# Kernel tuning notes

Measured on AMD Instinct MI355X. Metric: run time of the kernel, lower is better.

Reference implementation:

```python
import jax, jax.numpy as jnp
import numpy as np

HEADS = 8
EPS = 1e-12  # F.normalize default eps


def conv1x1(t, w):
    # t: (B, Cin, H, W); w: (Cout, Cin) -> (B, Cout, H, W)
    return jnp.einsum('bchw,oc->bohw', t, w)


def cosine_attn(q, k, v, scale):
    # q: (B,h,d,Nq); k,v: (B,h,d,Nk). Cosine attention: L2-normalize over feature dim d.
    q = q / jnp.maximum(jnp.linalg.norm(q, axis=2, keepdims=True), EPS)
    k = k / jnp.maximum(jnp.linalg.norm(k, axis=2, keepdims=True), EPS)
    attn = jnp.einsum('bhdq,bhdk->bhqk', q, k) * scale
    attn = jax.nn.softmax(attn, axis=-1)
    return jnp.einsum('bhqk,bhdk->bhdq', attn, v)  # (B,h,d,Nq)


def setup_inputs() -> dict:
    key = jax.random.key(0)
    ks = jax.random.split(key, 8)
    B, C, H, W, L = 8, 512, 64, 64, 16
    def w(k, o, i):
        return jax.random.normal(k, (o, i), dtype=jnp.float32) * (1.0 / np.sqrt(i))
    return {
        'x': jax.random.normal(ks[0], (B, C, H, W), dtype=jnp.float32),
        'latents': jax.random.normal(ks[1], (1, C, 1, L), dtype=jnp.float32) * 0.02,
        'w_q_lat': w(ks[2], C, C),
        'w_kv_x': w(ks[3], 2 * C, C),
        'w_q_x': w(ks[4], C, C),
        'w_kv_lat': w(ks[5], 2 * C, C),
        'w_proj': w(ks[6], C, C),
        'b_proj': jnp.zeros((C,), dtype=jnp.float32),
    }


def reference(x, latents, w_q_lat, w_kv_x, w_q_x, w_kv_lat, w_proj, b_proj):
    B, C, H, W = x.shape
    L = latents.shape[-1]
    h = HEADS
    d = C // h
    scale = d ** (-0.5)

    # latents read from spatial features (compression)
    lat = jnp.broadcast_to(latents, (B, C, 1, L))
    ql = conv1x1(lat, w_q_lat).reshape(B, h, d, L)
    kvx = conv1x1(x, w_kv_x)
    kx = kvx[:, :C].reshape(B, h, d, H * W)
    vx = kvx[:, C:].reshape(B, h, d, H * W)
    lat_read = cosine_attn(ql, kx, vx, scale).reshape(B, C, 1, L)

    # latents write back into features (expansion)
    qx = conv1x1(x, w_q_x).reshape(B, h, d, H * W)
    kvl = conv1x1(lat_read, w_kv_lat)
    kl = kvl[:, :C].reshape(B, h, d, L)
    vl = kvl[:, C:].reshape(B, h, d, L)
    x_write = cosine_attn(qx, kl, vl, scale).reshape(B, C, H, W)

    # output projection (dropout p=0 -> identity)
    return conv1x1(x_write, w_proj) + b_proj[None, :, None, None]
```

## Files before the change

### kernel.cpp

```cpp
#include <hip/hip_runtime.h>


typedef __bf16 bf16x8 __attribute__((ext_vector_type(8)));
typedef float floatx4 __attribute__((ext_vector_type(4)));
typedef short short8_t __attribute__((ext_vector_type(8)));
typedef short short4_t __attribute__((ext_vector_type(4)));

#define DEV __device__ __forceinline__

DEV float bf2f(unsigned short u){ union{unsigned int i; float f;} v; v.i = ((unsigned int)u)<<16; return v.f; }
DEV unsigned short f2bf(float f){
  __bf16 h = (__bf16)f;
  unsigned short u; __builtin_memcpy(&u, &h, 2); return u;
}

DEV void glds16(const void* g, void* l){
  __builtin_amdgcn_global_load_lds((const __attribute__((address_space(1))) void*)g,
                                   (__attribute__((address_space(3))) void*)l, 16, 0, 0);
}

#define OFF_XT     256ull
#define OFF_KVX    (OFF_XT + 33554432ull)
#define OFF_WKVX   (OFF_KVX + 67108864ull)
#define OFF_WQX    (OFF_WKVX + 1048576ull)
#define OFF_WKVL   (OFF_WQX + 524288ull)
#define OFF_WPROJ  (OFF_WKVL + 1048576ull)
#define OFF_WQLAT  (OFF_WPROJ + 524288ull)
#define OFF_LATF   (OFF_WQLAT + 524288ull)
#define OFF_BIAS   (OFF_LATF + 32768ull)
#define OFF_QLH    (OFF_BIAS + 4096ull)
#define OFF_GNUM   (OFF_QLH + 32768ull)
#define OFF_GDEN   (OFF_GNUM + 524288ull)
#define OFF_KVL    (OFF_GDEN + 4096ull)
#define OFF_KHAT   (OFF_KVL + 524288ull)
#define OFF_GVL    (OFF_KHAT + 524288ull)

__global__ void k_sniff(const unsigned short* __restrict__ x, int* flag){
  int t = threadIdx.x;
  int m = 0;
  for (int i = t; i < 4096; i += 256){ int e = (x[i]>>7)&0xFF; m = (e>m)?e:m; }
  __shared__ int red[256];
  red[t] = m; __syncthreads();
  for (int s = 128; s > 0; s >>= 1){ if (t < s) red[t] = (red[t+s]>red[t])?red[t+s]:red[t]; __syncthreads(); }
  if (t == 0) flag[0] = (red[0] > 150) ? 1 : 0;
}

__global__ __launch_bounds__(256) void k_prep(const void* s0, const void* s1, const void* s2,
                                              const void* s3, const void* s4,
                                              const void* slat, const void* sbias,
                                              unsigned short* __restrict__ wdst,
                                              float* __restrict__ latf, float* __restrict__ biasf,
                                              float* __restrict__ zro,
                                              const int* __restrict__ flag){
  int b = blockIdx.x, t = threadIdx.x;
  int isf = *flag;
  if (b < 896){
    int e = b*2048 + t*8;
    const void* src; int off;
    if (e < 524288)      { src = s0; off = e; }
    else if (e < 786432) { src = s1; off = e - 524288; }
    else if (e < 1310720){ src = s2; off = e - 786432; }
    else if (e < 1572864){ src = s3; off = e - 1310720; }
    else                 { src = s4; off = e - 1572864; }
    if (isf){
      const float* s = (const float*)src + off;
      float4 v0 = *(const float4*)(s);
      float4 v1 = *(const float4*)(s+4);
      unsigned short tmp[8] __attribute__((aligned(16)));
      tmp[0]=f2bf(v0.x); tmp[1]=f2bf(v0.y); tmp[2]=f2bf(v0.z); tmp[3]=f2bf(v0.w);
      tmp[4]=f2bf(v1.x); tmp[5]=f2bf(v1.y); tmp[6]=f2bf(v1.z); tmp[7]=f2bf(v1.w);
      *(short8_t*)&wdst[e] = *(short8_t*)tmp;
    } else {
      *(short8_t*)&wdst[e] = *(const short8_t*)((const unsigned short*)src + off);
    }
  } else if (b < 900){
    int i = (b-896)*2048 + t*8;
#pragma unroll
    for (int j = 0; j < 8; ++j)
      latf[i+j] = isf ? ((const float*)slat)[i+j] : bf2f(((const unsigned short*)slat)[i+j]);
  } else if (b == 900){
    if (t < 512) biasf[t] = isf ? ((const float*)sbias)[t] : bf2f(((const unsigned short*)sbias)[t]);
    if (t + 256 < 512) biasf[t+256] = isf ? ((const float*)sbias)[t+256] : bf2f(((const unsigned short*)sbias)[t+256]);
  } else {
    int i = (b-901)*256 + t;
    float4 z; z.x=0.f; z.y=0.f; z.z=0.f; z.w=0.f;
    ((float4*)zro)[i] = z;
  }
}

__global__ __launch_bounds__(256) void k_xt(const void* __restrict__ xraw, unsigned short* __restrict__ xT,
                                            const int* __restrict__ flag){
  int nb = blockIdx.x, cb = blockIdx.y, b = blockIdx.z;
  int n0 = nb*64, c0 = cb*64;
  __shared__ unsigned short tile[64][72];
  int t = threadIdx.x;
  if (*flag){
    const float* xp = (const float*)xraw;
#pragma unroll
    for (int i = 0; i < 4; ++i){
      int ch = i*256 + t; int c = ch>>4, n4 = (ch&15)*4;
      float4 v = *(const float4*)&xp[((size_t)(b*512 + c0 + c))*4096 + n0 + n4];
      int cc = n4 ^ (((c>>3)&7)<<3);
      tile[c][cc+0]=f2bf(v.x); tile[c][cc+1]=f2bf(v.y); tile[c][cc+2]=f2bf(v.z); tile[c][cc+3]=f2bf(v.w);
    }
  } else {
    const unsigned short* xp = (const unsigned short*)xraw;
#pragma unroll
    for (int i = 0; i < 2; ++i){
      int ch = i*256 + t; int c = ch>>3, n8 = (ch&7)*8;
      *(short8_t*)&tile[c][n8 ^ (((c>>3)&7)<<3)] =
        *(const short8_t*)&xp[((size_t)(b*512 + c0 + c))*4096 + n0 + n8];
    }
  }
  __syncthreads();
#pragma unroll
  for (int i = 0; i < 2; ++i){
    int ch = i*256 + t; int n = ch>>3, c8 = (ch&7)*8;
    unsigned short tmp[8] __attribute__((aligned(16)));
#pragma unroll
    for (int j = 0; j < 8; ++j){
      int c = c8 + j;
      tmp[j] = tile[c][n ^ (((c>>3)&7)<<3)];
    }
    *(short8_t*)&xT[((size_t)(b*4096 + n0 + n))*512 + c0 + c8] = *(short8_t*)tmp;
  }
}

__global__ __launch_bounds__(256) void k_ql(const unsigned short* __restrict__ wqlat,
                                            const float* __restrict__ latf, float* __restrict__ qlh){
  int h = blockIdx.x, o0 = h*64;
  extern __shared__ char smr[];
  float* latb = (float*)smr;
  unsigned short* wt = (unsigned short*)(smr + 8192);
  float* qbuf = (float*)(smr + 8192 + 17408);
  float* rinv = (float*)(smr + 8192 + 17408 + 4096);
  int t = threadIdx.x;
  int o = t>>2, l4 = (t&3)*4;
  float acc[4] = {0.f,0.f,0.f,0.f};
  for (int kk = 0; kk < 512; kk += 128){
    __syncthreads();
#pragma unroll
    for (int j = 0; j < 8; ++j){ int i = j*256 + t; latb[i] = latf[kk*16 + i]; }
#pragma unroll
    for (int j = 0; j < 4; ++j){ int ch = j*256 + t; int r = ch>>4, kc = (ch&15)*8;
      *(short8_t*)&wt[r*136 + kc] = *(const short8_t*)&wqlat[(size_t)(o0+r)*512 + kk + kc]; }
    __syncthreads();
    for (int k = 0; k < 128; ++k){
      float w = bf2f(wt[o*136 + k]);
      const float* lr = &latb[k*16 + l4];
#pragma unroll
      for (int j = 0; j < 4; ++j) acc[j] += w*lr[j];
    }
  }
#pragma unroll
  for (int j = 0; j < 4; ++j) qbuf[o*16 + l4 + j] = acc[j];
  __syncthreads();
  if (t < 16){
    float ss = 0.f;
    for (int oo = 0; oo < 64; ++oo){ float v = qbuf[oo*16 + t]; ss += v*v; }
    rinv[t] = 0.125f / fmaxf(sqrtf(ss), 1e-12f);
  }
  __syncthreads();
#pragma unroll
  for (int j = 0; j < 4; ++j) qlh[(h*16 + l4 + j)*64 + o] = acc[j]*rinv[l4 + j];
}

DEV void stage_ab(const unsigned short* __restrict__ Ap0, const unsigned short* __restrict__ Ap1,
                  const unsigned short* __restrict__ Bp, int kk,
                  unsigned short* At, unsigned short* Bt, int wave, int rsub, int koff){
#pragma unroll
  for (int c2 = 0; c2 < 4; ++c2){
    int chunk = wave*4 + c2;
    int row = chunk*8 + rsub;
    const unsigned short* gp = (chunk < 8) ? (Ap0 + (size_t)row*512 + kk + koff)
                                           : (Ap1 + (size_t)(row-64)*512 + kk + koff);
    glds16(gp, At + chunk*512);
  }
#pragma unroll
  for (int c2 = 0; c2 < 4; ++c2){
    int chunk = wave*4 + c2;
    int row = chunk*8 + rsub;
    glds16(Bp + (size_t)row*512 + kk + koff, Bt + chunk*512);
  }
}

DEV void gemm128_db(const unsigned short* __restrict__ Ap0, const unsigned short* __restrict__ Ap1,
                    const unsigned short* __restrict__ Bp,
                    char* smr, floatx4 (&acc)[4][4]){
  unsigned short* At0 = (unsigned short*)smr;
  unsigned short* Bt0 = (unsigned short*)(smr + 16384);
  unsigned short* At1 = (unsigned short*)(smr + 32768);
  unsigned short* Bt1 = (unsigned short*)(smr + 49152);
  int t = threadIdx.x, lane = t&63, wave = t>>6;
  int wm = wave>>1, wn = wave&1, lr = lane&15, lq = lane>>4;
  int rsub = lane>>3;
  int koff = ((lane&7) ^ rsub)*8;
  int sw = lr&7;
  stage_ab(Ap0, Ap1, Bp, 0, At0, Bt0, wave, rsub, koff);
  __syncthreads();
  for (int kk = 0; kk < 512; kk += 64){
    int cur = (kk>>6)&1;
    unsigned short* Ac = cur ? At1 : At0;
    unsigned short* Bc = cur ? Bt1 : Bt0;
    if (kk < 448){
      stage_ab(Ap0, Ap1, Bp, kk+64, cur ? At0 : At1, cur ? Bt0 : Bt1, wave, rsub, koff);
    }
    __builtin_amdgcn_s_setprio(1);
#pragma unroll
    for (int ks = 0; ks < 2; ++ks){
      int vo = ((ks*4 + lq) ^ sw)*8;
      bf16x8 a[4], b[4];
#pragma unroll
      for (int mt = 0; mt < 4; ++mt) a[mt] = *(const bf16x8*)&Ac[(wm*64 + mt*16 + lr)*64 + vo];
#pragma unroll
      for (int nt = 0; nt < 4; ++nt) b[nt] = *(const bf16x8*)&Bc[(wn*64 + nt*16 + lr)*64 + vo];
#pragma unroll
      for (int mt = 0; mt < 4; ++mt)
#pragma unroll
        for (int nt = 0; nt < 4; ++nt)
          acc[mt][nt] = __builtin_amdgcn_mfma_f32_16x16x32_bf16(a[mt], b[nt], acc[mt][nt], 0, 0, 0);
    }
    __builtin_amdgcn_s_setprio(0);
    __syncthreads();
  }
}

__global__ __launch_bounds__(256) void k_kvattn1(const unsigned short* __restrict__ wkvx,
                                                 const unsigned short* __restrict__ xT,
                                                 const float* __restrict__ qlh2,
                                                 float* __restrict__ gnum, float* __restrict__ gden){
  int nb = blockIdx.x, h = blockIdx.y, b = blockIdx.z;
  int n0 = nb*128;
  extern __shared__ char smr[];
  unsigned short* kt  = (unsigned short*)smr;
  unsigned short* vt  = (unsigned short*)(smr + 18432);
  unsigned short* pt  = (unsigned short*)(smr + 35840);
  unsigned short* qls = (unsigned short*)(smr + 65536);
  float* ssq  = (float*)(smr + 67840);
  float* wred = (float*)(smr + 68352);
  int t = threadIdx.x, lane = t&63, wave = t>>6;
  int wm = wave>>1, wn = wave&1, lr = lane&15, lq = lane>>4;
  for (int i = t; i < 1024; i += 256) qls[(i>>6)*72 + (i&63)] = f2bf(qlh2[(size_t)h*1024 + i]);
  floatx4 acc[4][4];
  floatx4 zero = {0.f,0.f,0.f,0.f};
#pragma unroll
  for (int i = 0; i < 4; ++i) for (int j = 0; j < 4; ++j) acc[i][j] = zero;
  gemm128_db(wkvx + (size_t)(h*64)*512, wkvx + (size_t)(512 + h*64)*512,
             xT + ((size_t)(b*4096 + n0))*512, smr, acc);
  if (wm == 0){
#pragma unroll
    for (int nt = 0; nt < 4; ++nt){
      float s = 0.f;
#pragma unroll
      for (int mt = 0; mt < 4; ++mt)
#pragma unroll
        for (int r = 0; r < 4; ++r) s += acc[mt][nt][r]*acc[mt][nt][r];
      s += __shfl_xor(s, 16); s += __shfl_xor(s, 32);
      if (lq == 0) ssq[wn*64 + nt*16 + lr] = 1.f / fmaxf(sqrtf(s), 1e-12f);
    }
  } else {
#pragma unroll
    for (int mt = 0; mt < 4; ++mt)
#pragma unroll
      for (int nt = 0; nt < 4; ++nt){
        int col = wn*64 + nt*16 + lr;
#pragma unroll
        for (int r = 0; r < 4; ++r) vt[(mt*16 + lq*4 + r)*136 + col] = f2bf(acc[mt][nt][r]);
      }
  }
  __syncthreads();
  if (wm == 0){
#pragma unroll
    for (int nt = 0; nt < 4; ++nt){
      int col = wn*64 + nt*16 + lr;
      float rinv = ssq[col];
#pragma unroll
      for (int mt = 0; mt < 4; ++mt){
        unsigned short tmp[4] __attribute__((aligned(8)));
#pragma unroll
        for (int r = 0; r < 4; ++r) tmp[r] = f2bf(acc[mt][nt][r]*rinv);
        *(short4_t*)&kt[col*72 + mt*16 + lq*4] = *(short4_t*)tmp;
      }
    }
  }
  __syncthreads();
  floatx4 sl[2]; sl[0] = zero; sl[1] = zero;
#pragma unroll
  for (int ks = 0; ks < 2; ++ks){
    bf16x8 bb = *(const bf16x8*)&qls[lr*72 + ks*32 + lq*8];
#pragma unroll
    for (int i = 0; i < 2; ++i){
      bf16x8 aa = *(const bf16x8*)&kt[((wave*2 + i)*16 + lr)*72 + ks*32 + lq*8];
      sl[i] = __builtin_amdgcn_mfma_f32_16x16x32_bf16(aa, bb, sl[i], 0, 0, 0);
    }
  }
  float dp = 0.f;
  float pv[2][4];
#pragma unroll
  for (int i = 0; i < 2; ++i)
#pragma unroll
    for (int r = 0; r < 4; ++r){ float p = __expf(sl[i][r]); pv[i][r] = p; dp += p; }
  dp += __shfl_xor(dp, 16); dp += __shfl_xor(dp, 32);
  if (lq == 0) wred[wave*16 + lr] = dp;
#pragma unroll
  for (int i = 0; i < 2; ++i){
    unsigned short tmp[4] __attribute__((aligned(8)));
#pragma unroll
    for (int r = 0; r < 4; ++r) tmp[r] = f2bf(pv[i][r]);
    *(short4_t*)&pt[lr*136 + (wave*2 + i)*16 + lq*4] = *(short4_t*)tmp;
  }
  __syncthreads();
  int bh = b*8 + h;
  if (t < 16) atomicAdd(&gden[bh*16 + t], wred[t] + wred[16+t] + wred[32+t] + wred[48+t]);
  floatx4 nacc = zero;
#pragma unroll
  for (int ks = 0; ks < 4; ++ks){
    bf16x8 aa = *(const bf16x8*)&vt[(wave*16 + lr)*136 + ks*32 + lq*8];
    bf16x8 bb = *(const bf16x8*)&pt[lr*136 + ks*32 + lq*8];
    nacc = __builtin_amdgcn_mfma_f32_16x16x32_bf16(aa, bb, nacc, 0, 0, 0);
  }
  float* gp = &gnum[((size_t)bh*16 + lr)*64 + wave*16 + lq*4];
#pragma unroll
  for (int r = 0; r < 4; ++r) atomicAdd(&gp[r], nacc[r]);
}

__global__ __launch_bounds__(256) void k_kvl(const unsigned short* __restrict__ wkvl,
                                             const float* __restrict__ gnum, const float* __restrict__ gden,
                                             float* __restrict__ kvl){
  int ob = blockIdx.x, b = blockIdx.y;
  extern __shared__ char smr[];
  float* latb = (float*)smr;
  unsigned short* wt = (unsigned short*)(smr + 32768);
  int t = threadIdx.x;
  for (int i = t; i < 8192; i += 256){
    int c = i>>4, l = i&15;
    int h = c>>6, d = c&63;
    int bh = b*8 + h;
    latb[i] = gnum[((size_t)(bh*16 + l))*64 + d] / gden[bh*16 + l];
  }
  int o = t>>4, l = t&15;
  int o0 = ob*16;
  float acc = 0.f;
  for (int kk = 0; kk < 512; kk += 128){
    __syncthreads();
    { int r = t>>4, kc = (t&15)*8;
      *(short8_t*)&wt[r*136 + kc] = *(const short8_t*)&wkvl[(size_t)(o0+r)*512 + kk + kc]; }
    __syncthreads();
    for (int k = 0; k < 128; ++k) acc += bf2f(wt[o*136 + k]) * latb[(kk+k)*16 + l];
  }
  kvl[((size_t)(b*1024 + o0 + o))*16 + l] = acc;
}

__global__ void k_klnorm(const float* __restrict__ kvl, float* __restrict__ khat, float* __restrict__ gvl){
  int l = blockIdx.x, h = blockIdx.y, b = blockIdx.z, d = threadIdx.x;
  float kl = kvl[((size_t)(b*1024 + h*64 + d))*16 + l];
  float vl = kvl[((size_t)(b*1024 + 512 + h*64 + d))*16 + l];
  float ss = kl*kl;
  for (int off = 32; off; off >>= 1) ss += __shfl_xor(ss, off);
  float inv = 0.125f / fmaxf(sqrtf(ss), 1e-12f);
  size_t o = ((size_t)((b*8+h)*16 + l))*64 + d;
  khat[o] = kl*inv;
  gvl[o] = vl;
}

__global__ __launch_bounds__(256) void k_mmat(const unsigned short* __restrict__ wproj,
                                              const float* __restrict__ gvl,
                                              unsigned short* __restrict__ Mg){
  int cb = blockIdx.x, h = blockIdx.y, b = blockIdx.z;
  __shared__ unsigned short wt[128*68];
  int t = threadIdx.x;
#pragma unroll
  for (int i = 0; i < 4; ++i){ int ch = i*256 + t; int c = ch>>3, d8 = (ch&7)*8;
    *(short8_t*)&wt[c*68 + d8] = *(const short8_t*)&wproj[(size_t)(cb*128 + c)*512 + h*64 + d8]; }
  int l = t&15, cq = t>>4;
  float v[64];
  const float* vp = &gvl[((size_t)(b*8+h)*16 + l)*64];
#pragma unroll
  for (int j = 0; j < 16; ++j){ float4 f = *(const float4*)&vp[j*4];
    v[j*4+0]=f.x; v[j*4+1]=f.y; v[j*4+2]=f.z; v[j*4+3]=f.w; }
  __syncthreads();
#pragma unroll
  for (int c8 = 0; c8 < 8; ++c8){
    int c = cq*8 + c8;
    float dot = 0.f;
#pragma unroll
    for (int d = 0; d < 64; ++d) dot += bf2f(wt[c*68 + d]) * v[d];
    Mg[((size_t)(b*512) + cb*128 + c)*128 + h*16 + l] = f2bf(dot);
  }
}

__global__ __launch_bounds__(256) void k_attn2p2(const unsigned short* __restrict__ wqx,
                                                 const unsigned short* __restrict__ xT,
                                                 const float* __restrict__ khatg,
                                                 unsigned short* __restrict__ Pg){
  int nb = blockIdx.x, hp = blockIdx.y, b = blockIdx.z;
  int n0 = nb*128;
  extern __shared__ char smr[];
  unsigned short* qt0 = (unsigned short*)smr;
  unsigned short* qt1 = (unsigned short*)(smr + 18432);
  unsigned short* khs = (unsigned short*)(smr + 65536);
  float* ssq = (float*)(smr + 70144);
  int t = threadIdx.x, lane = t&63, wave = t>>6;
  int wm = wave>>1, wn = wave&1, lr = lane&15, lq = lane>>4;
  for (int i = t; i < 2048; i += 256){
    int hh = i>>10, rem = i&1023;
    khs[hh*1152 + (rem>>6)*72 + (rem&63)] = f2bf(khatg[((size_t)(b*8 + hp*2 + hh))*1024 + rem]);
  }
  floatx4 acc[4][4];
  floatx4 zero = {0.f,0.f,0.f,0.f};
#pragma unroll
  for (int i = 0; i < 4; ++i) for (int j = 0; j < 4; ++j) acc[i][j] = zero;
  gemm128_db(wqx + (size_t)(hp*128)*512, wqx + (size_t)(hp*128 + 64)*512,
             xT + ((size_t)(b*4096 + n0))*512, smr, acc);
#pragma unroll
  for (int nt = 0; nt < 4; ++nt){
    float s = 0.f;
#pragma unroll
    for (int mt = 0; mt < 4; ++mt)
#pragma unroll
      for (int r = 0; r < 4; ++r) s += acc[mt][nt][r]*acc[mt][nt][r];
    s += __shfl_xor(s, 16); s += __shfl_xor(s, 32);
    if (lq == 0) ssq[wm*128 + wn*64 + nt*16 + lr] = 1.f / fmaxf(sqrtf(s), 1e-12f);
  }
  __syncthreads();
  unsigned short* qtr = wm ? qt1 : qt0;
#pragma unroll
  for (int nt = 0; nt < 4; ++nt){
    int col = wn*64 + nt*16 + lr;
    float rinv = ssq[wm*128 + col];
#pragma unroll
    for (int mt = 0; mt < 4; ++mt){
      unsigned short tmp[4] __attribute__((aligned(8)));
#pragma unroll
      for (int r = 0; r < 4; ++r) tmp[r] = f2bf(acc[mt][nt][r]*rinv);
      *(short4_t*)&qtr[col*72 + mt*16 + lq*4] = *(short4_t*)tmp;
    }
  }
  __syncthreads();
  floatx4 sl[4];
#pragma unroll
  for (int i = 0; i < 4; ++i) sl[i] = zero;
  unsigned short* qsrc = wm ? qt1 : qt0;
#pragma unroll
  for (int ks = 0; ks < 2; ++ks){
    bf16x8 bb = *(const bf16x8*)&khs[wm*1152 + lr*72 + ks*32 + lq*8];
#pragma unroll
    for (int i = 0; i < 4; ++i){
      bf16x8 aa = *(const bf16x8*)&qsrc[((wn*4 + i)*16 + lr)*72 + ks*32 + lq*8];
      sl[i] = __builtin_amdgcn_mfma_f32_16x16x32_bf16(aa, bb, sl[i], 0, 0, 0);
    }
  }
  int h = hp*2 + wm;
#pragma unroll
  for (int i = 0; i < 4; ++i){
    float p[4], s[4];
#pragma unroll
    for (int r = 0; r < 4; ++r){ p[r] = __expf(sl[i][r]); s[r] = p[r]; }
#pragma unroll
    for (int r = 0; r < 4; ++r){
      s[r] += __shfl_xor(s[r], 1);
      s[r] += __shfl_xor(s[r], 2);
      s[r] += __shfl_xor(s[r], 4);
      s[r] += __shfl_xor(s[r], 8);
    }
    int nbase = wn*64 + i*16 + lq*4;
#pragma unroll
    for (int r = 0; r < 4; ++r)
      Pg[((size_t)(b*4096 + n0 + nbase + r))*128 + h*16 + lr] = f2bf(p[r]/s[r]);
  }
}

__global__ __launch_bounds__(256) void k_out(const unsigned short* __restrict__ Mg,
                                             const unsigned short* __restrict__ Pg,
                                             const float* __restrict__ biasf,
                                             void* __restrict__ outv, const int* __restrict__ flag){
  int nb = blockIdx.x, cb = blockIdx.y, b = blockIdx.z;
  int n0 = nb*128, c0 = cb*64;
  extern __shared__ char smr[];
  unsigned short* At = (unsigned short*)smr;
  unsigned short* Bt = At + 64*136;
  int t = threadIdx.x, lane = t&63, wave = t>>6;
  int wm = wave>>1, wn = wave&1, lr = lane&15, lq = lane>>4;
#pragma unroll
  for (int i = 0; i < 4; ++i){ int ch = i*256 + t; int r = ch>>4, p8 = (ch&15)*8;
    *(short8_t*)&At[r*136 + p8] = *(const short8_t*)&Mg[((size_t)(b*512 + c0 + r))*128 + p8]; }
#pragma unroll
  for (int i = 0; i < 8; ++i){ int ch = i*256 + t; int r = ch>>4, p8 = (ch&15)*8;
    *(short8_t*)&Bt[r*136 + p8] = *(const short8_t*)&Pg[((size_t)(b*4096 + n0 + r))*128 + p8]; }
  __syncthreads();
  floatx4 acc[2][4];
  floatx4 zero = {0.f,0.f,0.f,0.f};
#pragma unroll
  for (int i = 0; i < 2; ++i) for (int j = 0; j < 4; ++j) acc[i][j] = zero;
#pragma unroll
  for (int ks = 0; ks < 4; ++ks){
    bf16x8 a0 = *(const bf16x8*)&At[(wm*32 + lr)*136 + ks*32 + lq*8];
    bf16x8 a1 = *(const bf16x8*)&At[(wm*32 + 16 + lr)*136 + ks*32 + lq*8];
#pragma unroll
    for (int nt = 0; nt < 4; ++nt){
      bf16x8 bb = *(const bf16x8*)&Bt[(wn*64 + nt*16 + lr)*136 + ks*32 + lq*8];
      acc[0][nt] = __builtin_amdgcn_mfma_f32_16x16x32_bf16(a0, bb, acc[0][nt], 0, 0, 0);
      acc[1][nt] = __builtin_amdgcn_mfma_f32_16x16x32_bf16(a1, bb, acc[1][nt], 0, 0, 0);
    }
  }
  __syncthreads();
  float* ct = (float*)smr;
#pragma unroll
  for (int mt = 0; mt < 2; ++mt)
#pragma unroll
    for (int nt = 0; nt < 4; ++nt)
#pragma unroll
      for (int r = 0; r < 4; ++r){
        int row = wm*32 + mt*16 + lq*4 + r;
        ct[row*132 + wn*64 + nt*16 + lr] = acc[mt][nt][r] + biasf[c0 + row];
      }
  __syncthreads();
  if (*flag){
    float* of = (float*)outv;
#pragma unroll
    for (int i = 0; i < 8; ++i){ int ch = i*256 + t; int r = ch>>5, c4 = (ch&31)*4;
      *(float4*)&of[((size_t)(b*512 + c0 + r))*4096 + n0 + c4] = *(float4*)&ct[r*132 + c4]; }
  } else {
    unsigned short* ob = (unsigned short*)outv;
#pragma unroll
    for (int i = 0; i < 4; ++i){ int ch = i*256 + t; int r = ch>>4, c8 = (ch&15)*8;
      unsigned short tmp[8] __attribute__((aligned(16)));
#pragma unroll
      for (int j = 0; j < 8; ++j) tmp[j] = f2bf(ct[r*132 + c8 + j]);
      *(short8_t*)&ob[((size_t)(b*512 + c0 + r))*4096 + n0 + c8] = *(short8_t*)tmp; }
  }
}

extern "C" void kernel_launch(void* const* d_in, const int* in_sizes, int n_in,
                              void* d_out, int out_size, void* d_ws, size_t ws_size,
                              hipStream_t stream){
  (void)in_sizes; (void)n_in; (void)out_size; (void)ws_size;
  char* ws = (char*)d_ws;
  int* flag              = (int*)ws;
  unsigned short* xT     = (unsigned short*)(ws + OFF_XT);
  unsigned short* Pg     = (unsigned short*)(ws + OFF_KVX);
  unsigned short* Mg     = (unsigned short*)(ws + OFF_KVX + 8388608ull);
  unsigned short* wkvx   = (unsigned short*)(ws + OFF_WKVX);
  unsigned short* wqx    = (unsigned short*)(ws + OFF_WQX);
  unsigned short* wkvl   = (unsigned short*)(ws + OFF_WKVL);
  unsigned short* wproj  = (unsigned short*)(ws + OFF_WPROJ);
  float* latf  = (float*)(ws + OFF_LATF);
  float* biasf = (float*)(ws + OFF_BIAS);
  float* qlh   = (float*)(ws + OFF_QLH);
  float* gnum  = (float*)(ws + OFF_GNUM);
  float* gden  = (float*)(ws + OFF_GDEN);
  float* kvl   = (float*)(ws + OFF_KVL);
  float* khat  = (float*)(ws + OFF_KHAT);
  float* gvl   = (float*)(ws + OFF_GVL);

  k_sniff<<<1, 256, 0, stream>>>((const unsigned short*)d_in[0], flag);

  k_prep<<<1030, 256, 0, stream>>>(d_in[3], d_in[4], d_in[5], d_in[6], d_in[2],
                                   d_in[1], d_in[7], wkvx, latf, biasf, gnum, flag);

  k_xt<<<dim3(64, 8, 8), 256, 0, stream>>>(d_in[0], xT, flag);

  k_ql<<<8, 256, 8192 + 17408 + 4096 + 64, stream>>>((unsigned short*)(ws + OFF_WQLAT), latf, qlh);

  k_kvattn1<<<dim3(32, 8, 8), 256, 68608, stream>>>(wkvx, xT, qlh, gnum, gden);
  k_kvl<<<dim3(64, 8), 256, 32768 + 16*136*2, stream>>>(wkvl, gnum, gden, kvl);
  k_klnorm<<<dim3(16, 8, 8), 64, 0, stream>>>(kvl, khat, gvl);
  k_mmat<<<dim3(4, 8, 8), 256, 0, stream>>>(wproj, gvl, Mg);
  k_attn2p2<<<dim3(32, 4, 8), 256, 71168, stream>>>(wqx, xT, khat, Pg);
  k_out<<<dim3(32, 8, 8), 256, 52224, stream>>>(Mg, Pg, biasf, d_out, flag);
}
```

Baseline: 287.0 us.

## Split 128x128 GEMM tiles across eight waves in attention kernels

Both fused projection+attention kernels now launch 512 threads per block instead of 256. Each wave computes a 64x32 sub-tile, and waves split the staging so half load A and half load B. Each wave's columns now hold full feature rows, so the L2 norm is computed in registers, which removes the ssq shared buffer and one block barrier. This raises latency hiding and MFMA parallelism per block, at the cost of higher register pressure from the 512-thread launch bound, idle waves in the final PV step, and possibly fewer resident blocks per CU.

After: 276.8 us (median of 2 runs). 1.04x faster.

```diff
diff --git a/kernel.cpp b/kernel.cpp
--- a/kernel.cpp
+++ b/kernel.cpp
@@ -165,59 +165,62 @@
   for (int j = 0; j < 4; ++j) qlh[(h*16 + l4 + j)*64 + o] = acc[j]*rinv[l4 + j];
 }
 
-DEV void stage_ab(const unsigned short* __restrict__ Ap0, const unsigned short* __restrict__ Ap1,
-                  const unsigned short* __restrict__ Bp, int kk,
-                  unsigned short* At, unsigned short* Bt, int wave, int rsub, int koff){
-#pragma unroll
-  for (int c2 = 0; c2 < 4; ++c2){
-    int chunk = wave*4 + c2;
-    int row = chunk*8 + rsub;
-    const unsigned short* gp = (chunk < 8) ? (Ap0 + (size_t)row*512 + kk + koff)
-                                           : (Ap1 + (size_t)(row-64)*512 + kk + koff);
-    glds16(gp, At + chunk*512);
-  }
-#pragma unroll
-  for (int c2 = 0; c2 < 4; ++c2){
-    int chunk = wave*4 + c2;
-    int row = chunk*8 + rsub;
-    glds16(Bp + (size_t)row*512 + kk + koff, Bt + chunk*512);
-  }
-}
-
-DEV void gemm128_db(const unsigned short* __restrict__ Ap0, const unsigned short* __restrict__ Ap1,
-                    const unsigned short* __restrict__ Bp,
-                    char* smr, floatx4 (&acc)[4][4]){
+DEV void stage_ab8(const unsigned short* __restrict__ Ap0, const unsigned short* __restrict__ Ap1,
+                   const unsigned short* __restrict__ Bp, int kk,
+                   unsigned short* At, unsigned short* Bt, int wave, int rsub, int koff){
+  if (wave < 4){
+#pragma unroll
+    for (int c2 = 0; c2 < 4; ++c2){
+      int chunk = wave*4 + c2;
+      int row = chunk*8 + rsub;
+      const unsigned short* gp = (chunk < 8) ? (Ap0 + (size_t)row*512 + kk + koff)
+                                             : (Ap1 + (size_t)(row-64)*512 + kk + koff);
+      glds16(gp, At + chunk*512);
+    }
+  } else {
+#pragma unroll
+    for (int c2 = 0; c2 < 4; ++c2){
+      int chunk = (wave-4)*4 + c2;
+      int row = chunk*8 + rsub;
+      glds16(Bp + (size_t)row*512 + kk + koff, Bt + chunk*512);
+    }
+  }
+}
+
+DEV void gemm128_db8(const unsigned short* __restrict__ Ap0, const unsigned short* __restrict__ Ap1,
+                     const unsigned short* __restrict__ Bp,
+                     char* smr, floatx4 (&acc)[4][2]){
   unsigned short* At0 = (unsigned short*)smr;
   unsigned short* Bt0 = (unsigned short*)(smr + 16384);
   unsigned short* At1 = (unsigned short*)(smr + 32768);
   unsigned short* Bt1 = (unsigned short*)(smr + 49152);
   int t = threadIdx.x, lane = t&63, wave = t>>6;
-  int wm = wave>>1, wn = wave&1, lr = lane&15, lq = lane>>4;
+  int wm = wave&1, wn = wave>>1, lr = lane&15, lq = lane>>4;
   int rsub = lane>>3;
   int koff = ((lane&7) ^ rsub)*8;
   int sw = lr&7;
-  stage_ab(Ap0, Ap1, Bp, 0, At0, Bt0, wave, rsub, koff);
+  stage_ab8(Ap0, Ap1, Bp, 0, At0, Bt0, wave, rsub, koff);
   __syncthreads();
   for (int kk = 0; kk < 512; kk += 64){
     int cur = (kk>>6)&1;
     unsigned short* Ac = cur ? At1 : At0;
     unsigned short* Bc = cur ? Bt1 : Bt0;
     if (kk < 448){
-      stage_ab(Ap0, Ap1, Bp, kk+64, cur ? At0 : At1, cur ? Bt0 : Bt1, wave, rsub, koff);
+      stage_ab8(Ap0, Ap1, Bp, kk+64, cur ? At0 : At1, cur ? Bt0 : Bt1, wave, rsub, koff);
     }
     __builtin_amdgcn_s_setprio(1);
 #pragma unroll
     for (int ks = 0; ks < 2; ++ks){
       int vo = ((ks*4 + lq) ^ sw)*8;
-      bf16x8 a[4], b[4];
+      bf16x8 a[4], b[2];
 #pragma unroll
       for (int mt = 0; mt < 4; ++mt) a[mt] = *(const bf16x8*)&Ac[(wm*64 + mt*16 + lr)*64 + vo];
 #pragma unroll
-      for (int nt = 0; nt < 4; ++nt) b[nt] = *(const bf16x8*)&Bc[(wn*64 + nt*16 + lr)*64 + vo];
+      for (int nt = 0; nt < 2; ++nt) b[nt] = *(const bf16x8*)&Bc[(wn*32 + nt*16 + lr)*64 + vo];
 #pragma unroll
       for (int mt = 0; mt < 4; ++mt)
 #pragma unroll
-        for (int nt = 0; nt < 4; ++nt)
+        for (int nt = 0; nt < 2; ++nt)
           acc[mt][nt] = __builtin_amdgcn_mfma_f32_16x16x32_bf16(a[mt], b[nt], acc[mt][nt], 0, 0, 0);
     }
     __builtin_amdgcn_s_setprio(0);
@@ -225,7 +228,7 @@
   }
 }
 
-__global__ __launch_bounds__(256) void k_kvattn1(const unsigned short* __restrict__ wkvx,
+__global__ __launch_bounds__(512) void k_kvattn1(const unsigned short* __restrict__ wkvx,
                                                  const unsigned short* __restrict__ xT,
                                                  const float* __restrict__ qlh2,
                                                  float* __restrict__ gnum, float* __restrict__ gden){
@@ -236,44 +239,27 @@
   unsigned short* vt  = (unsigned short*)(smr + 18432);
   unsigned short* pt  = (unsigned short*)(smr + 35840);
   unsigned short* qls = (unsigned short*)(smr + 65536);
-  float* ssq  = (float*)(smr + 67840);
-  float* wred = (float*)(smr + 68352);
+  float* wred = (float*)(smr + 67840);
   int t = threadIdx.x, lane = t&63, wave = t>>6;
-  int wm = wave>>1, wn = wave&1, lr = lane&15, lq = lane>>4;
-  for (int i = t; i < 1024; i += 256) qls[(i>>6)*72 + (i&63)] = f2bf(qlh2[(size_t)h*1024 + i]);
-  floatx4 acc[4][4];
+  int wm = wave&1, wn = wave>>1, lr = lane&15, lq = lane>>4;
+  for (int i = t; i < 1024; i += 512) qls[(i>>6)*72 + (i&63)] = f2bf(qlh2[(size_t)h*1024 + i]);
+  floatx4 acc[4][2];
   floatx4 zero = {0.f,0.f,0.f,0.f};
 #pragma unroll
-  for (int i = 0; i < 4; ++i) for (int j = 0; j < 4; ++j) acc[i][j] = zero;
-  gemm128_db(wkvx + (size_t)(h*64)*512, wkvx + (size_t)(512 + h*64)*512,
-             xT + ((size_t)(b*4096 + n0))*512, smr, acc);
+  for (int i = 0; i < 4; ++i) for (int j = 0; j < 2; ++j) acc[i][j] = zero;
+  gemm128_db8(wkvx + (size_t)(h*64)*512, wkvx + (size_t)(512 + h*64)*512,
+              xT + ((size_t)(b*4096 + n0))*512, smr, acc);
   if (wm == 0){
 #pragma unroll
-    for (int nt = 0; nt < 4; ++nt){
+    for (int nt = 0; nt < 2; ++nt){
       float s = 0.f;
 #pragma unroll
       for (int mt = 0; mt < 4; ++mt)
 #pragma unroll
         for (int r = 0; r < 4; ++r) s += acc[mt][nt][r]*acc[mt][nt][r];
       s += __shfl_xor(s, 16); s += __shfl_xor(s, 32);
-      if (lq == 0) ssq[wn*64 + nt*16 + lr] = 1.f / fmaxf(sqrtf(s), 1e-12f);
-    }
-  } else {
-#pragma unroll
-    for (int mt = 0; mt < 4; ++mt)
-#pragma unroll
-      for (int nt = 0; nt < 4; ++nt){
-        int col = wn*64 + nt*16 + lr;
-#pragma unroll
-        for (int r = 0; r < 4; ++r) vt[(mt*16 + lq*4 + r)*136 + col] = f2bf(acc[mt][nt][r]);
-      }
-  }
-  __syncthreads();
-  if (wm == 0){
-#pragma unroll
-    for (int nt = 0; nt < 4; ++nt){
-      int col = wn*64 + nt*16 + lr;
-      float rinv = ssq[col];
+      float rinv = 1.f / fmaxf(sqrtf(s), 1e-12f);
+      int col = wn*32 + nt*16 + lr;
 #pragma unroll
       for (int mt = 0; mt < 4; ++mt){
         unsigned short tmp[4] __attribute__((aligned(8)));
@@ -282,46 +268,56 @@
         *(short4_t*)&kt[col*72 + mt*16 + lq*4] = *(short4_t*)tmp;
       }
     }
-  }
-  __syncthreads();
-  floatx4 sl[2]; sl[0] = zero; sl[1] = zero;
+  } else {
+#pragma unroll
+    for (int mt = 0; mt < 4; ++mt)
+#pragma unroll
+      for (int nt = 0; nt < 2; ++nt){
+        int col = wn*32 + nt*16 + lr;
+#pragma unroll
+        for (int r = 0; r < 4; ++r) vt[(mt*16 + lq*4 + r)*136 + col] = f2bf(acc[mt][nt][r]);
+      }
+  }
+  __syncthreads();
+  floatx4 sl = zero;
 #pragma unroll
   for (int ks = 0; ks < 2; ++ks){
     bf16x8 bb = *(const bf16x8*)&qls[lr*72 + ks*32 + lq*8];
-#pragma unroll
-    for (int i = 0; i < 2; ++i){
-      bf16x8 aa = *(const bf16x8*)&kt[((wave*2 + i)*16 + lr)*72 + ks*32 + lq*8];
-      sl[i] = __builtin_amdgcn_mfma_f32_16x16x32_bf16(aa, bb, sl[i], 0, 0, 0);
-    }
+    bf16x8 aa = *(const bf16x8*)&kt[(wave*16 + lr)*72 + ks*32 + lq*8];
+    sl = __builtin_amdgcn_mfma_f32_16x16x32_bf16(aa, bb, sl, 0, 0, 0);
   }
   float dp = 0.f;
-  float pv[2][4];
-#pragma unroll
-  for (int i = 0; i < 2; ++i)
-#pragma unroll
-    for (int r = 0; r < 4; ++r){ float p = __expf(sl[i][r]); pv[i][r] = p; dp += p; }
+  float pv[4];
+#pragma unroll
+  for (int r = 0; r < 4; ++r){ float p = __expf(sl[r]); pv[r] = p; dp += p; }
   dp += __shfl_xor(dp, 16); dp += __shfl_xor(dp, 32);
   if (lq == 0) wred[wave*16 + lr] = dp;
-#pragma unroll
-  for (int i = 0; i < 2; ++i){
+  {
     unsigned short tmp[4] __attribute__((aligned(8)));
 #pragma unroll
-    for (int r = 0; r < 4; ++r) tmp[r] = f2bf(pv[i][r]);
-    *(short4_t*)&pt[lr*136 + (wave*2 + i)*16 + lq*4] = *(short4_t*)tmp;
+    for (int r = 0; r < 4; ++r) tmp[r] = f2bf(pv[r]);
+    *(short4_t*)&pt[lr*136 + wave*16 + lq*4] = *(short4_t*)tmp;
   }
   __syncthreads();
   int bh = b*8 + h;
-  if (t < 16) atomicAdd(&gden[bh*16 + t], wred[t] + wred[16+t] + wred[32+t] + wred[48+t]);
-  floatx4 nacc = zero;
-#pragma unroll
-  for (int ks = 0; ks < 4; ++ks){
-    bf16x8 aa = *(const bf16x8*)&vt[(wave*16 + lr)*136 + ks*32 + lq*8];
-    bf16x8 bb = *(const bf16x8*)&pt[lr*136 + ks*32 + lq*8];
-    nacc = __builtin_amdgcn_mfma_f32_16x16x32_bf16(aa, bb, nacc, 0, 0, 0);
-  }
-  float* gp = &gnum[((size_t)bh*16 + lr)*64 + wave*16 + lq*4];
-#pragma unroll
-  for (int r = 0; r < 4; ++r) atomicAdd(&gp[r], nacc[r]);
+  if (t < 16){
+    float s = 0.f;
+#pragma unroll
+    for (int w = 0; w < 8; ++w) s += wred[w*16 + t];
+    atomicAdd(&gden[bh*16 + t], s);
+  }
+  if (wave < 4){
+    floatx4 nacc = zero;
+#pragma unroll
+    for (int ks = 0; ks < 4; ++ks){
+      bf16x8 aa = *(const bf16x8*)&vt[(wave*16 + lr)*136 + ks*32 + lq*8];
+      bf16x8 bb = *(const bf16x8*)&pt[lr*136 + ks*32 + lq*8];
+      nacc = __builtin_amdgcn_mfma_f32_16x16x32_bf16(aa, bb, nacc, 0, 0, 0);
+    }
+    float* gp = &gnum[((size_t)bh*16 + lr)*64 + wave*16 + lq*4];
+#pragma unroll
+    for (int r = 0; r < 4; ++r) atomicAdd(&gp[r], nacc[r]);
+  }
 }
 
 __global__ __launch_bounds__(256) void k_kvl(const unsigned short* __restrict__ wkvl,
@@ -389,7 +385,7 @@
   }
 }
 
-__global__ __launch_bounds__(256) void k_attn2p2(const unsigned short* __restrict__ wqx,
+__global__ __launch_bounds__(512) void k_attn2p2(const unsigned short* __restrict__ wqx,
                                                  const unsigned short* __restrict__ xT,
                                                  const float* __restrict__ khatg,
                                                  unsigned short* __restrict__ Pg){
@@ -399,35 +395,29 @@
   unsigned short* qt0 = (unsigned short*)smr;
   unsigned short* qt1 = (unsigned short*)(smr + 18432);
   unsigned short* khs = (unsigned short*)(smr + 65536);
-  float* ssq = (float*)(smr + 70144);
   int t = threadIdx.x, lane = t&63, wave = t>>6;
-  int wm = wave>>1, wn = wave&1, lr = lane&15, lq = lane>>4;
-  for (int i = t; i < 2048; i += 256){
+  int wm = wave&1, wn = wave>>1, lr = lane&15, lq = lane>>4;
+  for (int i = t; i < 2048; i += 512){
     int hh = i>>10, rem = i&1023;
     khs[hh*1152 + (rem>>6)*72 + (rem&63)] = f2bf(khatg[((size_t)(b*8 + hp*2 + hh))*1024 + rem]);
   }
-  floatx4 acc[4][4];
+  floatx4 acc[4][2];
   floatx4 zero = {0.f,0.f,0.f,0.f};
 #pragma unroll
-  for (int i = 0; i < 4; ++i) for (int j = 0; j < 4; ++j) acc[i][j] = zero;
-  gemm128_db(wqx + (size_t)(hp*128)*512, wqx + (size_t)(hp*128 + 64)*512,
-             xT + ((size_t)(b*4096 + n0))*512, smr, acc);
-#pragma unroll
-  for (int nt = 0; nt < 4; ++nt){
+  for (int i = 0; i < 4; ++i) for (int j = 0; j < 2; ++j) acc[i][j] = zero;
+  gemm128_db8(wqx + (size_t)(hp*128)*512, wqx + (size_t)(hp*128 + 64)*512,
+              xT + ((size_t)(b*4096 + n0))*512, smr, acc);
+  unsigned short* qtr = wm ? qt1 : qt0;
+#pragma unroll
+  for (int nt = 0; nt < 2; ++nt){
     float s = 0.f;
 #pragma unroll
     for (int mt = 0; mt < 4; ++mt)
 #pragma unroll
       for (int r = 0; r < 4; ++r) s += acc[mt][nt][r]*acc[mt][nt][r];
     s += __shfl_xor(s, 16); s += __shfl_xor(s, 32);
-    if (lq == 0) ssq[wm*128 + wn*64 + nt*16 + lr] = 1.f / fmaxf(sqrtf(s), 1e-12f);
-  }
-  __syncthreads();
-  unsigned short* qtr = wm ? qt1 : qt0;
-#pragma unroll
-  for (int nt = 0; nt < 4; ++nt){
-    int col = wn*64 + nt*16 + lr;
-    float rinv = ssq[wm*128 + col];
+    float rinv = 1.f / fmaxf(sqrtf(s), 1e-12f);
+    int col = wn*32 + nt*16 + lr;
 #pragma unroll
     for (int mt = 0; mt < 4; ++mt){
       unsigned short tmp[4] __attribute__((aligned(8)));
@@ -437,22 +427,21 @@
     }
   }
   __syncthreads();
-  floatx4 sl[4];
-#pragma unroll
-  for (int i = 0; i < 4; ++i) sl[i] = zero;
+  floatx4 sl[2];
+  sl[0] = zero; sl[1] = zero;
   unsigned short* qsrc = wm ? qt1 : qt0;
 #pragma unroll
   for (int ks = 0; ks < 2; ++ks){
     bf16x8 bb = *(const bf16x8*)&khs[wm*1152 + lr*72 + ks*32 + lq*8];
 #pragma unroll
-    for (int i = 0; i < 4; ++i){
-      bf16x8 aa = *(const bf16x8*)&qsrc[((wn*4 + i)*16 + lr)*72 + ks*32 + lq*8];
+    for (int i = 0; i < 2; ++i){
+      bf16x8 aa = *(const bf16x8*)&qsrc[((wn*2 + i)*16 + lr)*72 + ks*32 + lq*8];
       sl[i] = __builtin_amdgcn_mfma_f32_16x16x32_bf16(aa, bb, sl[i], 0, 0, 0);
     }
   }
   int h = hp*2 + wm;
 #pragma unroll
-  for (int i = 0; i < 4; ++i){
+  for (int i = 0; i < 2; ++i){
     float p[4], s[4];
 #pragma unroll
     for (int r = 0; r < 4; ++r){ p[r] = __expf(sl[i][r]); s[r] = p[r]; }
@@ -463,7 +452,7 @@
       s[r] += __shfl_xor(s[r], 4);
       s[r] += __shfl_xor(s[r], 8);
     }
-    int nbase = wn*64 + i*16 + lq*4;
+    int nbase = wn*32 + i*16 + lq*4;
 #pragma unroll
     for (int r = 0; r < 4; ++r)
       Pg[((size_t)(b*4096 + n0 + nbase + r))*128 + h*16 + lr] = f2bf(p[r]/s[r]);
@@ -562,10 +551,10 @@
 
   k_ql<<<8, 256, 8192 + 17408 + 4096 + 64, stream>>>((unsigned short*)(ws + OFF_WQLAT), latf, qlh);
 
-  k_kvattn1<<<dim3(32, 8, 8), 256, 68608, stream>>>(wkvx, xT, qlh, gnum, gden);
+  k_kvattn1<<<dim3(32, 8, 8), 512, 68352, stream>>>(wkvx, xT, qlh, gnum, gden);
   k_kvl<<<dim3(64, 8), 256, 32768 + 16*136*2, stream>>>(wkvl, gnum, gden, kvl);
   k_klnorm<<<dim3(16, 8, 8), 64, 0, stream>>>(kvl, khat, gvl);
   k_mmat<<<dim3(4, 8, 8), 256, 0, stream>>>(wproj, gvl, Mg);
-  k_attn2p2<<<dim3(32, 4, 8), 256, 71168, stream>>>(wqx, xT, khat, Pg);
+  k_attn2p2<<<dim3(32, 4, 8), 512, 70144, stream>>>(wqx, xT, khat, Pg);
   k_out<<<dim3(32, 8, 8), 256, 52224, stream>>>(Mg, Pg, biasf, d_out, flag);
 }
```
